# Kernel optimization log

Hardware: AMD Instinct MI355X
Metric: run time of the kernel (lower is better)

## Reference

```python
import jax, jax.numpy as jnp
import numpy as np

B, T, N1, N2, D, H, DH = 8, 4, 1024, 64, 1024, 16, 64
INNER = H * DH
EPS = 1e-5


def layernorm(x, g, b):
    mu = jnp.mean(x, axis=-1, keepdims=True)
    var = jnp.var(x, axis=-1, keepdims=True)
    return (x - mu) * jax.lax.rsqrt(var + EPS) * g + b


def setup_inputs() -> dict:
    key = jax.random.key(0)
    ks = jax.random.split(key, 8)
    s = 0.02
    return {
        "x": jax.random.normal(ks[0], (B, T, N1, D), jnp.float32),
        "latents": jax.random.normal(ks[1], (B, T, N2, D), jnp.float32),
        "gm": jnp.ones((D,), jnp.float32),
        "bm": jnp.zeros((D,), jnp.float32),
        "gl": jnp.ones((D,), jnp.float32),
        "bl": jnp.zeros((D,), jnp.float32),
        "Wq": jax.random.normal(ks[2], (D, INNER), jnp.float32) * s,
        "Wkv": jax.random.normal(ks[3], (D, 2 * INNER), jnp.float32) * s,
        "Wout": jax.random.normal(ks[4], (INNER, D), jnp.float32) * s,
        "Wd1": jax.random.normal(ks[5], (D, D // 4), jnp.float32) * s,
        "bd1": jnp.zeros((D // 4,), jnp.float32),
        "Wd2": jax.random.normal(ks[6], (D // 4, H), jnp.float32) * s,
        "bd2": jnp.zeros((H,), jnp.float32),
    }


def reference(x, latents, gm, bm, gl, bl, Wq, Wkv, Wout, Wd1, bd1, Wd2, bd2):
    b, t, n1, d = x.shape
    n2 = latents.shape[2]
    h, dh = H, DH
    scale = dh ** -0.5

    xn = layernorm(x, gm, bm)
    ln = layernorm(latents, gl, bl)

    # q: (b, h, t, n2, dh)
    q = (ln @ Wq).reshape(b, t, n2, h, dh).transpose(0, 3, 1, 2, 4)
    # kv over image tokens + first latent token -> nk = n1 + 1
    kv_in = jnp.concatenate([xn, ln[:, :, 0:1]], axis=2)
    nk = n1 + 1
    kv = (kv_in @ Wkv).reshape(b, t, nk, 2, h, dh)
    k = kv[:, :, :, 0].transpose(0, 3, 1, 2, 4)  # (b, h, t, nk, dh)
    v = kv[:, :, :, 1].transpose(0, 3, 1, 2, 4)

    sim = jnp.einsum('bhtid,bhtjd->bhtij', q * scale, k)
    sim = sim - jax.lax.stop_gradient(jnp.max(sim, axis=-1, keepdims=True))
    attn = jax.nn.softmax(sim, axis=-1)

    # dynamic per-head weights from mean-pooled (normed) latents: (b, t, h)
    hid = jax.nn.relu(ln.mean(axis=2) @ Wd1 + bd1)
    dw = jax.nn.softmax(hid @ Wd2 + bd2, axis=-1)
    attn = attn * dw.transpose(0, 2, 1)[:, :, :, None, None]  # (b,h,t,1,1)

    out = jnp.einsum('bhtij,bhtjd->bhtid', attn, v)
    out = out.transpose(0, 2, 3, 1, 4).reshape(b, t, n2, h * dh)
    return out @ Wout
```

## Files before the change

kernel.cpp:

```cpp
#include <hip/hip_runtime.h>
#include <cstdint>
#include <cstddef>

constexpr int CB = 8, CT = 4, CN1 = 1024, CN2 = 64, CD = 1024, CH = 16, CDH = 64;
constexpr int CBT = CB * CT;
constexpr int CNK = CN1 + 1;
constexpr int CINNER = CH * CDH;

__device__ __forceinline__ unsigned short f2bf(float f) {
  union { float f; unsigned int u; } v; v.f = f;
  unsigned int u = v.u;
  u += 0x7fffu + ((u >> 16) & 1u);
  return (unsigned short)(u >> 16);
}

typedef __attribute__((ext_vector_type(8))) short short8;
typedef __attribute__((ext_vector_type(8))) __bf16 bf16x8;
typedef __attribute__((ext_vector_type(4))) float floatx4;

template <typename V>
__device__ __forceinline__ auto mfma_bf16_impl(V a, V b, floatx4 c, int)
    -> decltype(__builtin_amdgcn_mfma_f32_16x16x32_bf16(a, b, c, 0, 0, 0)) {
  return __builtin_amdgcn_mfma_f32_16x16x32_bf16(a, b, c, 0, 0, 0);
}
template <typename V>
__device__ __forceinline__ floatx4 mfma_bf16_impl(V a, V b, floatx4 c, long) {
  return __builtin_amdgcn_mfma_f32_16x16x32_bf16(
      __builtin_bit_cast(bf16x8, a), __builtin_bit_cast(bf16x8, b), c, 0, 0, 0);
}
__device__ __forceinline__ floatx4 mfma_bf16(short8 a, short8 b, floatx4 c) {
  return mfma_bf16_impl(a, b, c, 0);
}

#if __has_builtin(__builtin_amdgcn_global_load_lds)
#define HAS_GLDS 1
__device__ __forceinline__ void glds16(const unsigned short* g, unsigned short* l) {
  __builtin_amdgcn_global_load_lds(
      (const __attribute__((address_space(1))) void*)g,
      (__attribute__((address_space(3))) void*)l, 16, 0, 0);
}
#else
#define HAS_GLDS 0
#endif

__global__ __launch_bounds__(256) void ln_kernel(
    const float* __restrict__ x, const float* __restrict__ g,
    const float* __restrict__ b, unsigned short* __restrict__ obf,
    float* __restrict__ of32) {
  const int row = blockIdx.x * 4 + (threadIdx.x >> 6);
  const int lane = threadIdx.x & 63;
  const float4* xr = (const float4*)(x + (size_t)row * CD);
  float4 v[4];
#pragma unroll
  for (int k = 0; k < 4; ++k) v[k] = xr[lane + 64 * k];
  float s = 0.f, s2 = 0.f;
#pragma unroll
  for (int k = 0; k < 4; ++k) {
    s  += v[k].x + v[k].y + v[k].z + v[k].w;
    s2 += v[k].x*v[k].x + v[k].y*v[k].y + v[k].z*v[k].z + v[k].w*v[k].w;
  }
#pragma unroll
  for (int off = 32; off; off >>= 1) { s += __shfl_xor(s, off); s2 += __shfl_xor(s2, off); }
  const float mean = s * (1.0f / 1024.0f);
  const float var  = s2 * (1.0f / 1024.0f) - mean * mean;
  const float rstd = rsqrtf(var + 1e-5f);
#pragma unroll
  for (int k = 0; k < 4; ++k) {
    const float4 gv = ((const float4*)g)[lane + 64 * k];
    const float4 bv = ((const float4*)b)[lane + 64 * k];
    float4 y;
    y.x = (v[k].x - mean) * rstd * gv.x + bv.x;
    y.y = (v[k].y - mean) * rstd * gv.y + bv.y;
    y.z = (v[k].z - mean) * rstd * gv.z + bv.z;
    y.w = (v[k].w - mean) * rstd * gv.w + bv.w;
    ushort4 o; o.x = f2bf(y.x); o.y = f2bf(y.y); o.z = f2bf(y.z); o.w = f2bf(y.w);
    ((ushort4*)(obf + (size_t)row * CD))[lane + 64 * k] = o;
    if (of32) ((float4*)(of32 + (size_t)row * CD))[lane + 64 * k] = y;
  }
}

__global__ __launch_bounds__(256) void wtrans_kernel(
    const float* __restrict__ W, unsigned short* __restrict__ WT, int K, int N) {
  __shared__ float t[64][65];
  const int n0 = blockIdx.x * 64, k0 = blockIdx.y * 64;
  const int tid = threadIdx.x;
  const int kr = tid >> 4, ns = (tid & 15) * 4;
#pragma unroll
  for (int i = 0; i < 4; ++i) {
    const int k = kr + i * 16;
    const float4 v = *(const float4*)&W[(size_t)(k0 + k) * N + n0 + ns];
    t[k][ns + 0] = v.x; t[k][ns + 1] = v.y; t[k][ns + 2] = v.z; t[k][ns + 3] = v.w;
  }
  __syncthreads();
  const int n = tid >> 2, ks = (tid & 3) * 16;
#pragma unroll
  for (int c = 0; c < 4; ++c) {
    ushort4 o;
    o.x = f2bf(t[ks + c * 4 + 0][n]);
    o.y = f2bf(t[ks + c * 4 + 1][n]);
    o.z = f2bf(t[ks + c * 4 + 2][n]);
    o.w = f2bf(t[ks + c * 4 + 3][n]);
    *(ushort4*)&WT[(size_t)(n0 + n) * K + k0 + ks + c * 4] = o;
  }
}

template <bool A_KV, bool C_BF16>
__global__ __launch_bounds__(256) void gemm128_kernel(
    const unsigned short* __restrict__ A, const unsigned short* __restrict__ xn,
    const unsigned short* __restrict__ lnb, const unsigned short* __restrict__ BT,
    unsigned short* __restrict__ Cb, float* __restrict__ Cf,
    int M, int N, int K) {
  __shared__ __attribute__((aligned(16))) unsigned short As[128 * 32];
  __shared__ __attribute__((aligned(16))) unsigned short Bs[128 * 32];
  const int tid = threadIdx.x;
  const int col0 = blockIdx.x * 128, row0 = blockIdx.y * 128;
  const int srow = tid >> 2, skseg = (tid & 3) * 8;

  auto arow_ptr = [&](int grow) -> const unsigned short* {
    if (grow >= M) grow = M - 1;
    if (A_KV) {
      const int bt = grow / CNK, j = grow - bt * CNK;
      return (j < CN1) ? xn + ((size_t)(bt * CN1 + j)) * K + skseg
                       : lnb + ((size_t)(bt * CN2)) * K + skseg;
    }
    return A + (size_t)grow * K + skseg;
  };
  const unsigned short* a0 = arow_ptr(row0 + srow);
  const unsigned short* a1 = arow_ptr(row0 + 64 + srow);
  const unsigned short* b0 = BT + (size_t)(col0 + srow) * K + skseg;
  const unsigned short* b1 = BT + (size_t)(col0 + 64 + srow) * K + skseg;

  const int lane = tid & 63, wave = tid >> 6;
  const int wrow = (wave >> 1) * 64, wcol = (wave & 1) * 64;
  const int i16 = lane & 15, quad = lane >> 4;

  floatx4 acc[4][4] = {};
  for (int kt = 0; kt < K; kt += 32) {
    __syncthreads();
#if HAS_GLDS
    glds16(a0 + kt, &As[tid * 8]);
    glds16(a1 + kt, &As[2048 + tid * 8]);
    glds16(b0 + kt, &Bs[tid * 8]);
    glds16(b1 + kt, &Bs[2048 + tid * 8]);
#else
    *(uint4*)&As[tid * 8]        = *(const uint4*)(a0 + kt);
    *(uint4*)&As[2048 + tid * 8] = *(const uint4*)(a1 + kt);
    *(uint4*)&Bs[tid * 8]        = *(const uint4*)(b0 + kt);
    *(uint4*)&Bs[2048 + tid * 8] = *(const uint4*)(b1 + kt);
#endif
    __syncthreads();
    short8 af[4], bf[4];
#pragma unroll
    for (int ti = 0; ti < 4; ++ti)
      af[ti] = *(const short8*)&As[(wrow + ti * 16 + i16) * 32 + quad * 8];
#pragma unroll
    for (int tj = 0; tj < 4; ++tj)
      bf[tj] = *(const short8*)&Bs[(wcol + tj * 16 + i16) * 32 + quad * 8];
#pragma unroll
    for (int ti = 0; ti < 4; ++ti)
#pragma unroll
      for (int tj = 0; tj < 4; ++tj)
        acc[ti][tj] = mfma_bf16(af[ti], bf[tj], acc[ti][tj]);
  }
#pragma unroll
  for (int ti = 0; ti < 4; ++ti)
#pragma unroll
    for (int tj = 0; tj < 4; ++tj) {
      const int gc = col0 + wcol + tj * 16 + i16;
#pragma unroll
      for (int r = 0; r < 4; ++r) {
        const int gr = row0 + wrow + ti * 16 + quad * 4 + r;
        if (gr < M) {
          if (C_BF16) Cb[(size_t)gr * N + gc] = f2bf(acc[ti][tj][r]);
          else        Cf[(size_t)gr * N + gc] = acc[ti][tj][r];
        }
      }
    }
}

__global__ __launch_bounds__(256) void dw_kernel(
    const float* __restrict__ lnf, const float* __restrict__ Wd1,
    const float* __restrict__ bd1, const float* __restrict__ Wd2,
    const float* __restrict__ bd2, float* __restrict__ dw) {
  __shared__ float mean[CD];
  __shared__ float hid[256];
  __shared__ float lg[16];
  const int bt = blockIdx.x, tid = threadIdx.x;
  const float* base = lnf + (size_t)bt * CN2 * CD;
  for (int d = tid; d < CD; d += 256) {
    float s = 0.f;
    for (int r = 0; r < CN2; ++r) s += base[(size_t)r * CD + d];
    mean[d] = s * (1.0f / 64.0f);
  }
  __syncthreads();
  {
    float s = bd1[tid];
    for (int d = 0; d < CD; ++d) s += mean[d] * Wd1[(size_t)d * 256 + tid];
    hid[tid] = fmaxf(s, 0.0f);
  }
  __syncthreads();
  if (tid < 16) {
    float s = bd2[tid];
    for (int o = 0; o < 256; ++o) s += hid[o] * Wd2[o * 16 + tid];
    lg[tid] = s;
  }
  __syncthreads();
  if (tid < 16) {
    float mx = lg[0];
    for (int h = 1; h < 16; ++h) mx = fmaxf(mx, lg[h]);
    float sum = 0.f;
    for (int h = 0; h < 16; ++h) sum += __expf(lg[h] - mx);
    dw[bt * 16 + tid] = __expf(lg[tid] - mx) / sum;
  }
}

__global__ __launch_bounds__(256) void attn_kernel(
    const unsigned short* __restrict__ Q,
    const unsigned short* __restrict__ KV,
    const float* __restrict__ dw,
    unsigned short* __restrict__ AO) {
  __shared__ __attribute__((aligned(16))) unsigned short ks[2][64 * 72];
  __shared__ __attribute__((aligned(16))) unsigned short vt[2][64 * 72];
  const int bt = blockIdx.x >> 4, h = blockIdx.x & 15;
  const int tid = threadIdx.x;
  const int lane = tid & 63, wave = tid >> 6;
  const int i16 = lane & 15, quad = lane >> 4;
  const int wrow = wave * 16;

  const unsigned short* qbase =
      Q + ((size_t)(bt * 64 + wrow + i16)) * CINNER + h * 64;
  const short8 bq0 = *(const short8*)(qbase + quad * 8);
  const short8 bq1 = *(const short8*)(qbase + 32 + quad * 8);

  const int jrb = tid & 31, seg = tid >> 5;
  const int t_ = jrb & 15, hlf_ = jrb >> 4;
  const int vcol0 = ((t_ >> 2) << 3) + (t_ & 3) + 4 * hlf_;
  const unsigned short* kvb = KV + ((size_t)bt * CNK) * 2048 + h * 64 + seg * 8;

  uint4 kk[2], vv[2];
  auto load_tile = [&](int j0) {
#pragma unroll
    for (int c = 0; c < 2; ++c) {
      const int j = j0 + c * 32 + jrb;
      if (j < CNK) {
        const unsigned short* p = kvb + (size_t)j * 2048;
        kk[c] = *(const uint4*)p;
        vv[c] = *(const uint4*)(p + 1024);
      } else {
        kk[c] = make_uint4(0, 0, 0, 0);
        vv[c] = make_uint4(0, 0, 0, 0);
      }
    }
  };
  auto write_tile = [&](int buf) {
#pragma unroll
    for (int c = 0; c < 2; ++c) {
      const int jr = c * 32 + jrb;
      *(uint4*)&ks[buf][jr * 72 + seg * 8] = kk[c];
      const int vcol = c * 32 + vcol0;
      const unsigned int w[4] = {vv[c].x, vv[c].y, vv[c].z, vv[c].w};
#pragma unroll
      for (int p = 0; p < 4; ++p) {
        vt[buf][(seg * 8 + 2 * p + 0) * 72 + vcol] = (unsigned short)(w[p] & 0xffffu);
        vt[buf][(seg * 8 + 2 * p + 1) * 72 + vcol] = (unsigned short)(w[p] >> 16);
      }
    }
  };

  float l = 0.f;
  floatx4 O[4] = {{0,0,0,0}, {0,0,0,0}, {0,0,0,0}, {0,0,0,0}};
  const float expC = 0.18033688011112042f;

  load_tile(0);
  write_tile(0);
  constexpr int NT = 17;
  for (int t = 0; t < NT; ++t) {
    if (t + 1 < NT) load_tile((t + 1) * 64);
    __syncthreads();
    const int buf = t & 1;
    const unsigned short* ksb = ks[buf];
    const unsigned short* vtb = vt[buf];
#pragma unroll
    for (int c = 0; c < 2; ++c) {
      floatx4 s0 = {0,0,0,0}, s1 = {0,0,0,0};
      const short8 a00 = *(const short8*)&ksb[((2*c)   * 16 + i16) * 72 + quad * 8];
      const short8 a01 = *(const short8*)&ksb[((2*c)   * 16 + i16) * 72 + 32 + quad * 8];
      const short8 a10 = *(const short8*)&ksb[((2*c+1) * 16 + i16) * 72 + quad * 8];
      const short8 a11 = *(const short8*)&ksb[((2*c+1) * 16 + i16) * 72 + 32 + quad * 8];
      s0 = mfma_bf16(a00, bq0, s0); s0 = mfma_bf16(a01, bq1, s0);
      s1 = mfma_bf16(a10, bq0, s1); s1 = mfma_bf16(a11, bq1, s1);
      unsigned short pb0[4], pb1[4];
      if (t == NT - 1) {
#pragma unroll
        for (int r = 0; r < 4; ++r) {
          const int k0g = t * 64 + (2*c)   * 16 + quad * 4 + r;
          const int k1g = t * 64 + (2*c+1) * 16 + quad * 4 + r;
          const float p0 = (k0g < CNK) ? exp2f(s0[r] * expC) : 0.f;
          const float p1 = (k1g < CNK) ? exp2f(s1[r] * expC) : 0.f;
          l += p0 + p1;
          pb0[r] = f2bf(p0); pb1[r] = f2bf(p1);
        }
      } else {
#pragma unroll
        for (int r = 0; r < 4; ++r) {
          const float p0 = exp2f(s0[r] * expC);
          const float p1 = exp2f(s1[r] * expC);
          l += p0 + p1;
          pb0[r] = f2bf(p0); pb1[r] = f2bf(p1);
        }
      }
      const short8 bp = {
          (short)pb0[0], (short)pb0[1], (short)pb0[2], (short)pb0[3],
          (short)pb1[0], (short)pb1[1], (short)pb1[2], (short)pb1[3]};
#pragma unroll
      for (int dt = 0; dt < 4; ++dt) {
        const short8 av = *(const short8*)&vtb[(dt * 16 + i16) * 72 + c * 32 + quad * 8];
        O[dt] = mfma_bf16(av, bp, O[dt]);
      }
    }
    if (t + 1 < NT) write_tile((t + 1) & 1);
  }

  l += __shfl_xor(l, 16);
  l += __shfl_xor(l, 32);
  const float wsc = dw[bt * 16 + h] / l;
  unsigned short* obase = AO + ((size_t)(bt * 64 + wrow + i16)) * CINNER + h * 64;
#pragma unroll
  for (int dt = 0; dt < 4; ++dt)
#pragma unroll
    for (int r = 0; r < 4; ++r)
      obase[dt * 16 + quad * 4 + r] = f2bf(O[dt][r] * wsc);
}

extern "C" void kernel_launch(void* const* d_in, const int* in_sizes, int n_in,
                              void* d_out, int out_size, void* d_ws, size_t ws_size,
                              hipStream_t stream) {
  const float* x       = (const float*)d_in[0];
  const float* latents = (const float*)d_in[1];
  const float* gm  = (const float*)d_in[2];
  const float* bm  = (const float*)d_in[3];
  const float* gl  = (const float*)d_in[4];
  const float* bl  = (const float*)d_in[5];
  const float* Wq  = (const float*)d_in[6];
  const float* Wkv = (const float*)d_in[7];
  const float* Wout= (const float*)d_in[8];
  const float* Wd1 = (const float*)d_in[9];
  const float* bd1 = (const float*)d_in[10];
  const float* Wd2 = (const float*)d_in[11];
  const float* bd2 = (const float*)d_in[12];
  float* out = (float*)d_out;

  char* ws = (char*)d_ws;
  size_t off = 0;
  auto alloc = [&](size_t bytes) -> void* {
    void* p = ws + off;
    off += (bytes + 255) & ~(size_t)255;
    return p;
  };
  unsigned short* xn   = (unsigned short*)alloc((size_t)CBT * CN1 * CD * 2);
  unsigned short* kv   = (unsigned short*)alloc((size_t)CBT * CNK * 2048 * 2);
  float*          lnf  = (float*)        alloc((size_t)CBT * CN2 * CD * 4);
  unsigned short* lnb  = (unsigned short*)alloc((size_t)CBT * CN2 * CD * 2);
  unsigned short* wqT  = (unsigned short*)alloc((size_t)CD * CINNER * 2);
  unsigned short* wkvT = (unsigned short*)alloc((size_t)CD * 2 * CINNER * 2);
  unsigned short* woT  = (unsigned short*)alloc((size_t)CINNER * CD * 2);
  unsigned short* qb   = (unsigned short*)alloc((size_t)CBT * CN2 * CINNER * 2);
  unsigned short* aob  = (unsigned short*)alloc((size_t)CBT * CN2 * CINNER * 2);
  float*          dwp  = (float*)        alloc((size_t)CBT * CH * 4);
  if (off > ws_size) return;

  ln_kernel<<<CBT * CN1 / 4, 256, 0, stream>>>(x, gm, bm, xn, nullptr);
  ln_kernel<<<CBT * CN2 / 4, 256, 0, stream>>>(latents, gl, bl, lnb, lnf);
  wtrans_kernel<<<dim3(CINNER / 64, CD / 64), 256, 0, stream>>>(Wq, wqT, CD, CINNER);
  wtrans_kernel<<<dim3(2 * CINNER / 64, CD / 64), 256, 0, stream>>>(Wkv, wkvT, CD, 2 * CINNER);
  wtrans_kernel<<<dim3(CD / 64, CINNER / 64), 256, 0, stream>>>(Wout, woT, CINNER, CD);
  gemm128_kernel<false, true><<<dim3(1024 / 128, 2048 / 128), 256, 0, stream>>>(
      lnb, nullptr, nullptr, wqT, qb, nullptr, 2048, 1024, 1024);
  gemm128_kernel<true, true><<<dim3(2048 / 128, (CBT * CNK + 127) / 128), 256, 0, stream>>>(
      nullptr, xn, lnb, wkvT, kv, nullptr, CBT * CNK, 2048, 1024);
  dw_kernel<<<CBT, 256, 0, stream>>>(lnf, Wd1, bd1, Wd2, bd2, dwp);
  attn_kernel<<<CBT * CH, 256, 0, stream>>>(qb, kv, dwp, aob);
  gemm128_kernel<false, false><<<dim3(1024 / 128, 2048 / 128), 256, 0, stream>>>(
      aob, nullptr, nullptr, woT, nullptr, out, 2048, 1024, 1024);
}
```

Baseline: 560.3 us.

## Add 256x256 tiled KV GEMM with 4-stage pipeline and grid swizzle

Replaces the 128x128 KV projection GEMM, the largest matmul, with a new 256x256-tile kernel using 512 threads, a 4-deep shared-memory ring of asynchronous global-to-LDS loads, XOR-swizzled LDS layout and a blockIdx remap across groups of eight blocks. The larger tile raises arithmetic intensity and data reuse per load, and the deeper prefetch is meant to hide memory latency. The kernel uses 128 KB of LDS and 128 accumulator registers per thread, which may limit occupancy or cause spills.

```diff
diff --git a/kernel.cpp b/kernel.cpp
--- a/kernel.cpp
+++ b/kernel.cpp
@@ -174,6 +174,107 @@
           if (C_BF16) Cb[(size_t)gr * N + gc] = f2bf(acc[ti][tj][r]);
           else        Cf[(size_t)gr * N + gc] = acc[ti][tj][r];
         }
+      }
+    }
+}
+
+template <bool A_KV>
+__global__ __launch_bounds__(512, 2) void gemm256_kernel(
+    const unsigned short* __restrict__ A, const unsigned short* __restrict__ xn,
+    const unsigned short* __restrict__ lnb, const unsigned short* __restrict__ BT,
+    unsigned short* __restrict__ Cb,
+    int M, int N, int K, int nbN) {
+  __shared__ __attribute__((aligned(16))) unsigned short As[4 * 8192];
+  __shared__ __attribute__((aligned(16))) unsigned short Bs[4 * 8192];
+  const int tid = threadIdx.x;
+
+  const int raw = blockIdx.x;
+  const int cpx = gridDim.x >> 3;
+  const int virt = (raw & 7) * cpx + (raw >> 3);
+  const int mb = virt / nbN, nb = virt - mb * nbN;
+  const int row0 = mb * 256, col0 = nb * 256;
+
+  auto arow = [&](int grow) -> const unsigned short* {
+    if (grow >= M) grow = M - 1;
+    if (A_KV) {
+      const int bt = grow / CNK, j = grow - bt * CNK;
+      return (j < CN1) ? xn + ((size_t)(bt * CN1 + j)) * K
+                       : lnb + ((size_t)(bt * CN2)) * K;
+    }
+    return A + (size_t)grow * K;
+  };
+  const int c0 = tid, c1 = tid + 512;
+  const int rA0 = c0 >> 2, sA0 = (c0 & 3) ^ ((rA0 >> 1) & 3);
+  const int rA1 = c1 >> 2, sA1 = (c1 & 3) ^ ((rA1 >> 1) & 3);
+  const unsigned short* pA0 = arow(row0 + rA0) + sA0 * 8;
+  const unsigned short* pA1 = arow(row0 + rA1) + sA1 * 8;
+  const unsigned short* pB0 = BT + (size_t)(col0 + rA0) * K + sA0 * 8;
+  const unsigned short* pB1 = BT + (size_t)(col0 + rA1) * K + sA1 * 8;
+
+  auto stage = [&](int s) {
+    const int sb = (s & 3) * 8192;
+#if HAS_GLDS
+    glds16(pA0 + s * 32, &As[sb + tid * 8]);
+    glds16(pA1 + s * 32, &As[sb + 4096 + tid * 8]);
+    glds16(pB0 + s * 32, &Bs[sb + tid * 8]);
+    glds16(pB1 + s * 32, &Bs[sb + 4096 + tid * 8]);
+#else
+    *(uint4*)&As[sb + tid * 8]        = *(const uint4*)(pA0 + s * 32);
+    *(uint4*)&As[sb + 4096 + tid * 8] = *(const uint4*)(pA1 + s * 32);
+    *(uint4*)&Bs[sb + tid * 8]        = *(const uint4*)(pB0 + s * 32);
+    *(uint4*)&Bs[sb + 4096 + tid * 8] = *(const uint4*)(pB1 + s * 32);
+#endif
+  };
+
+  const int lane = tid & 63, wave = tid >> 6;
+  const int wr = wave >> 2, wc = wave & 3;
+  const int i16 = lane & 15, quad = lane >> 4;
+  int offA[8], offB[4];
+#pragma unroll
+  for (int ti = 0; ti < 8; ++ti) {
+    const int r = wr * 128 + ti * 16 + i16;
+    offA[ti] = r * 32 + (quad ^ ((r >> 1) & 3)) * 8;
+  }
+#pragma unroll
+  for (int tj = 0; tj < 4; ++tj) {
+    const int r = wc * 64 + tj * 16 + i16;
+    offB[tj] = r * 32 + (quad ^ ((r >> 1) & 3)) * 8;
+  }
+
+  floatx4 acc[8][4] = {};
+  const int NSL = K >> 5;
+  stage(0); stage(1); stage(2);
+
+  for (int s = 0; s < NSL; ++s) {
+    asm volatile("s_waitcnt vmcnt(8)" ::: "memory");
+    __builtin_amdgcn_s_barrier();
+    __builtin_amdgcn_sched_barrier(0);
+    const unsigned short* Asl = &As[(s & 3) * 8192];
+    const unsigned short* Bsl = &Bs[(s & 3) * 8192];
+    short8 af[8], bf[4];
+#pragma unroll
+    for (int ti = 0; ti < 8; ++ti) af[ti] = *(const short8*)(Asl + offA[ti]);
+#pragma unroll
+    for (int tj = 0; tj < 4; ++tj) bf[tj] = *(const short8*)(Bsl + offB[tj]);
+    if (s + 3 < NSL) stage(s + 3);
+    __builtin_amdgcn_s_setprio(1);
+#pragma unroll
+    for (int ti = 0; ti < 8; ++ti)
+#pragma unroll
+      for (int tj = 0; tj < 4; ++tj)
+        acc[ti][tj] = mfma_bf16(af[ti], bf[tj], acc[ti][tj]);
+    __builtin_amdgcn_s_setprio(0);
+  }
+
+#pragma unroll
+  for (int ti = 0; ti < 8; ++ti)
+#pragma unroll
+    for (int tj = 0; tj < 4; ++tj) {
+      const int gc = col0 + wc * 64 + tj * 16 + i16;
+#pragma unroll
+      for (int r = 0; r < 4; ++r) {
+        const int gr = row0 + wr * 128 + ti * 16 + quad * 4 + r;
+        if (gr < M) Cb[(size_t)gr * N + gc] = f2bf(acc[ti][tj][r]);
       }
     }
 }
@@ -376,8 +477,11 @@
   wtrans_kernel<<<dim3(CD / 64, CINNER / 64), 256, 0, stream>>>(Wout, woT, CINNER, CD);
   gemm128_kernel<false, true><<<dim3(1024 / 128, 2048 / 128), 256, 0, stream>>>(
       lnb, nullptr, nullptr, wqT, qb, nullptr, 2048, 1024, 1024);
-  gemm128_kernel<true, true><<<dim3(2048 / 128, (CBT * CNK + 127) / 128), 256, 0, stream>>>(
-      nullptr, xn, lnb, wkvT, kv, nullptr, CBT * CNK, 2048, 1024);
+  {
+    const int MB = (CBT * CNK + 255) / 256;
+    gemm256_kernel<true><<<MB * 8, 512, 0, stream>>>(
+        nullptr, xn, lnb, wkvT, kv, CBT * CNK, 2048, 1024, 8);
+  }
   dw_kernel<<<CBT, 256, 0, stream>>>(lnf, Wd1, bd1, Wd2, bd2, dwp);
   attn_kernel<<<CBT * CH, 256, 0, stream>>>(qb, kv, dwp, aob);
   gemm128_kernel<false, false><<<dim3(1024 / 128, 2048 / 128), 256, 0, stream>>>(
```

Result: faster. 541.5 us (-3.3%).
